# Optimization experiments

Measured on AMD Instinct MI355X. Metric: run time of the kernel, lower is better.

## Reference

```python
import jax, jax.numpy as jnp
import numpy as np

# --- LCAModel hyperparameters (from init_kwargs) ---
NUM_SIMS = 2048
NUM_DIM = 8
NUM_STEPS = 1500
THRESHOLD = 1.0
LEAK = 0.1
COMPETITION = 0.1
SELF_EXC = 0.0
NOISE_STD = 1.0
DT = 0.01
SQRT_STEP = float(np.sqrt(0.001))  # hardcoded in LCALayer (sqrt(0.001), not sqrt(DT))


def setup_inputs() -> dict:
    key = jax.random.key(0)
    inp = jax.random.uniform(key, (NUM_SIMS, NUM_DIM), dtype=jnp.float32)
    return {"input": inp}


def reference(input):
    B, D = input.shape
    # gamma: off-diagonal -competition, diagonal self_excitation
    gamma = jnp.full((D, D), -COMPETITION, dtype=input.dtype)
    gamma = gamma.at[jnp.diag_indices(D)].set(SELF_EXC)
    noise_key = jax.random.key(42)

    def step(carry, t):
        pre, act = carry
        # stop integrating once any accumulator crosses threshold
        active = jnp.all(jnp.abs(act) < THRESHOLD, axis=1, keepdims=True).astype(pre.dtype)
        # faithful to torch: sum(matmul(act, gamma), dim=1, keepdim=True) -> [B, 1]
        rec = jnp.sum(act @ gamma, axis=1, keepdims=True)
        pre = pre + (input - LEAK * pre + rec) * active * DT
        dw = active * NOISE_STD * jax.random.normal(
            jax.random.fold_in(noise_key, t), (B, D), dtype=pre.dtype)
        pre = pre + dw * SQRT_STEP
        act = jax.nn.relu(pre)
        return (pre, act), (pre, act)

    init = (jnp.zeros_like(input), jnp.zeros_like(input))
    _, (pre_traj, act_traj) = jax.lax.scan(step, init, jnp.arange(NUM_STEPS))
    # prepend the zero initial state and move time to the last axis: [B, D, T+1]
    zeros = jnp.zeros((1, B, D), input.dtype)
    pre_all = jnp.moveaxis(jnp.concatenate([zeros, pre_traj], axis=0), 0, -1)
    act_all = jnp.moveaxis(jnp.concatenate([zeros, act_traj], axis=0), 0, -1)
    return (pre_all, act_all)
```

## Files before the change

kernel.cpp:

```cpp
#include <hip/hip_runtime.h>
#include <stdint.h>

#define NSIMS 2048
#define NDIM 8
#define NE (NSIMS * NDIM)
#define NSTEPS 1500
#define TP1 (NSTEPS + 1)
#define TILE 64
#define NTILE ((NSTEPS + TILE - 1) / TILE)
#define SENT 0x7fffffff

__device__ __forceinline__ void tf_block(uint32_t k0, uint32_t k1,
                                         uint32_t x0, uint32_t x1,
                                         uint32_t& o0, uint32_t& o1) {
  const uint32_t k2 = k0 ^ k1 ^ 0x1BD11BDAu;
  x0 += k0; x1 += k1;
#define TF_R(r) { x0 += x1; x1 = (x1 << (r)) | (x1 >> (32 - (r))); x1 ^= x0; }
  TF_R(13) TF_R(15) TF_R(26) TF_R(6)
  x0 += k1; x1 += k2 + 1u;
  TF_R(17) TF_R(29) TF_R(16) TF_R(24)
  x0 += k2; x1 += k0 + 2u;
  TF_R(13) TF_R(15) TF_R(26) TF_R(6)
  x0 += k0; x1 += k1 + 3u;
  TF_R(17) TF_R(29) TF_R(16) TF_R(24)
  x0 += k1; x1 += k2 + 4u;
  TF_R(13) TF_R(15) TF_R(26) TF_R(6)
  x0 += k2; x1 += k0 + 5u;
#undef TF_R
  o0 = x0; o1 = x1;
}

__device__ __forceinline__ float bits_to_normal(uint32_t bits) {
#pragma clang fp contract(off)
  const float LO = -0.99999994f;
  float f = __uint_as_float((bits >> 9) | 0x3F800000u) - 1.0f;
  float u = f * 2.0f + LO;
  u = fmaxf(LO, u);
  float t = __builtin_fmaf(-u, u, 1.0f);
  float L = __log2f(t);
  float p;
  if (L > -7.2134752f) {
    float w = __builtin_fmaf(-0.69314718f, L, -2.5f);
    p = 3.97426059e-08f;
    p = 4.85462660e-07f + p * w;
    p = -4.98282379e-06f + p * w;
    p = -6.21053119e-06f + p * w;
    p = 3.09120051e-04f + p * w;
    p = -1.77303519e-03f + p * w;
    p = -5.90813402e-03f + p * w;
    p = 3.48802730e-01f + p * w;
    p = 2.12331454e+00f + p * w;
  } else {
    float w = sqrtf(-0.69314718f * L) - 3.0f;
    p = -2.83145880e-04f;
    p = 1.42765648e-04f + p * w;
    p = 1.90826058e-03f + p * w;
    p = -5.19501312e-03f + p * w;
    p = 8.11688966e-03f + p * w;
    p = -1.07797881e-02f + p * w;
    p = 1.33485786e-02f + p * w;
    p = 1.41658104e+00f + p * w;
    p = 4.00643424e+00f + p * w;
  }
  return p * u;
}

__global__ void k_fold(uint2* __restrict__ keys) {
  int t = blockIdx.x * blockDim.x + threadIdx.x;
  if (t >= NSTEPS) return;
  uint32_t o0, o1;
  tf_block(0u, 42u, 0u, (uint32_t)t, o0, o1);
  keys[t] = make_uint2(o0, o1);
}

template <int CTRL>
__device__ __forceinline__ float dppf(float v) {
  int r = __builtin_amdgcn_update_dpp(0, __builtin_bit_cast(int, v), CTRL, 0xF, 0xF, true);
  return __builtin_bit_cast(float, r);
}
template <int CTRL>
__device__ __forceinline__ int dppi(int v) {
  return __builtin_amdgcn_update_dpp(0, v, CTRL, 0xF, 0xF, true);
}

#define STEP(ST, NZ)                                                    \
  {                                                                     \
    _Pragma("clang fp contract(off)")                                   \
    float S = act;                                                      \
    S = S + dppf<0xB1>(S);                                              \
    S = S + dppf<0x4E>(S);                                              \
    S = S + dppf<0x141>(S);                                             \
    const float rec = (S * -0.1f) * 7.0f;   \
    float a_ = inp - 0.1f * pre;                                        \
    float b_ = a_ + rec;                                                \
    float cg = b_ * activeF;                                            \
    pre = pre + cg * 0.01f;                                             \
    float dwn = activeF * (NZ);                                         \
    pre = pre + dwn * 0.031622776601683793f; \
    act = fmaxf(pre, 0.0f);                                             \
    fc = (act >= 1.0f) ? (((ST) < fc) ? (ST) : fc) : fc;                \
    ptile[ST][lane] = pre;                                              \
  }

__global__ void __launch_bounds__(512, 2) k_fused(const float* __restrict__ input,
                                                  const uint2* __restrict__ keys,
                                                  float* __restrict__ out) {
  __shared__ float ring[2][TILE][64];
  __shared__ float ptile[TILE][65];
  __shared__ float spre[64];
  __shared__ int sfz;
  const int tid = threadIdx.x;
  const int wid = tid >> 6;
  const int lane = tid & 63;
  const int e0 = (int)blockIdx.x << 6;
  const int e = e0 + lane;
  const size_t actoff = (size_t)NE * TP1;

  if (tid == 0) sfz = SENT;

  float pre = 0.0f, act = 0.0f, activeF = 1.0f, inp = 0.0f;
  if (wid == 0) {
    inp = input[e];
    const size_t rowo = (size_t)e * TP1;
    out[rowo] = 0.0f;
    out[actoff + rowo] = 0.0f;
  } else {
    const int j0 = wid - 1;
    uint2 fk[10];
#pragma unroll
    for (int rr = 0; rr < 10; ++rr) {
      const int j = j0 + rr * 7;
      fk[rr] = (j < TILE) ? keys[j] : make_uint2(0u, 0u);
    }
#pragma unroll
    for (int rr = 0; rr < 10; ++rr) {
      const int j = j0 + rr * 7;
      if (j < TILE) {
        uint32_t o0, o1;
        tf_block(fk[rr].x, fk[rr].y, 0u, (uint32_t)e, o0, o1);
        ring[0][j][lane] = bits_to_normal(o0 ^ o1);
      }
    }
  }
  __syncthreads();

  int fz = SENT;
  for (int k = 0; k < NTILE; ++k) {
    const int par = k & 1;
    const int base = k * TILE;
    const int nst = (NSTEPS - base < TILE) ? (NSTEPS - base) : TILE;
    if (wid == 0) {
      int fc = TILE;
      if (nst == TILE) {
#pragma unroll
        for (int ch = 0; ch < 2; ++ch) {
          float nz[32];
#pragma unroll
          for (int j = 0; j < 32; ++j) nz[j] = ring[par][ch * 32 + j][lane];
#pragma unroll
          for (int j = 0; j < 32; ++j) STEP(ch * 32 + j, nz[j])
        }
      } else {
#pragma unroll
        for (int ch = 0; ch < 2; ++ch) {
          float nz[32];
#pragma unroll
          for (int j = 0; j < 32; ++j) nz[j] = ring[par][ch * 32 + j][lane];
#pragma unroll
          for (int j = 0; j < 32; ++j) {
            const int st = ch * 32 + j;
            if (st >= nst) break;
            STEP(st, nz[j])
          }
        }
      }
      int c = fc;
      { int t_ = dppi<0xB1>(c);  c = (t_ < c) ? t_ : c; }
      { int t_ = dppi<0x4E>(c);  c = (t_ < c) ? t_ : c; }
      { int t_ = dppi<0x141>(c); c = (t_ < c) ? t_ : c; }
      if (activeF > 0.0f && c < TILE) {
        const float fpre = ptile[c][lane];
        for (int s = c + 1; s < TILE; ++s) ptile[s][lane] = fpre;
        pre = fpre;
        act = fmaxf(fpre, 0.0f);
        activeF = 0.0f;
      }
      if (__ballot(activeF > 0.0f) == 0ull) {
        spre[lane] = pre;
        if (lane == 0) sfz = base + nst + 1;
      }
    } else {
      const int nb = base + TILE;
      const int j0 = wid - 1;
      uint2 fk[10];
#pragma unroll
      for (int rr = 0; rr < 10; ++rr) {
        const int j = j0 + rr * 7;
        const int t = nb + j;
        fk[rr] = (j < TILE && t < NSTEPS) ? keys[t] : make_uint2(0u, 0u);
      }
#pragma unroll
      for (int rr = 0; rr < 10; ++rr) {
        const int j = j0 + rr * 7;
        const int t = nb + j;
        if (j < TILE && t < NSTEPS) {
          uint32_t o0, o1;
          tf_block(fk[rr].x, fk[rr].y, 0u, (uint32_t)e, o0, o1);
          ring[par ^ 1][j][lane] = bits_to_normal(o0 ^ o1);
        }
      }
    }
    __syncthreads();
    if (lane < nst) {
      const int tau = base + 1 + lane;
#pragma unroll
      for (int ee = 0; ee < 8; ++ee) {
        const int el = (wid << 3) + ee;
        const float p = ptile[lane][el];
        const size_t o = (size_t)(e0 + el) * TP1 + (size_t)tau;
        out[o] = p;
        out[actoff + o] = fmaxf(p, 0.0f);
      }
    }
    if (sfz != SENT) { fz = sfz; break; }
    __syncthreads();
  }

  if (fz <= NSTEPS) {
#pragma unroll
    for (int ee = 0; ee < 8; ++ee) {
      const int el = (wid << 3) + ee;
      const float p = spre[el];
      const float a = fmaxf(p, 0.0f);
      const size_t ro = (size_t)(e0 + el) * TP1;
      for (int tau = fz + lane; tau <= NSTEPS; tau += 64) {
        out[ro + (size_t)tau] = p;
        out[actoff + ro + (size_t)tau] = a;
      }
    }
  }
}

extern "C" void kernel_launch(void* const* d_in, const int* in_sizes, int n_in,
                              void* d_out, int out_size, void* d_ws, size_t ws_size,
                              hipStream_t stream) {
  const float* input = (const float*)d_in[0];
  float* out = (float*)d_out;
  uint2* keys = (uint2*)d_ws;
  if (ws_size < NSTEPS * sizeof(uint2)) return;

  k_fold<<<dim3((NSTEPS + 255) / 256), dim3(256), 0, stream>>>(keys);
  k_fused<<<dim3(NSIMS / 8), dim3(512), 0, stream>>>(input, keys, out);
}
```

Baseline: 128.4 us.

## Double tile size, shorten reduction chain, and drop active-mask from recurrence

Raises the time tile from 64 to 128 steps, which halves the number of block-wide barriers and tile handoffs. The 8-lane sum is rebuilt as a shallower DPP tree with parallel adds, which shortens the serial dependency chain of each step. The active mask is removed from the per-step update: frozen lanes keep integrating, and the store phase overwrites their output with the frozen value using shared sfroz/spre flags. The noise-generation loops become rolled with a key prefetch, and the launch bound drops the minimum-2-blocks hint. The larger shared-memory footprint and the looser register limit may reduce occupancy, and the reordered additions may change rounding relative to the sequential sum.

```diff
diff --git a/kernel.cpp b/kernel.cpp
--- a/kernel.cpp
+++ b/kernel.cpp
@@ -6,7 +6,7 @@
 #define NE (NSIMS * NDIM)
 #define NSTEPS 1500
 #define TP1 (NSTEPS + 1)
-#define TILE 64
+#define TILE 128
 #define NTILE ((NSTEPS + TILE - 1) / TILE)
 #define SENT 0x7fffffff
 
@@ -86,28 +86,30 @@
 #define STEP(ST, NZ)                                                    \
   {                                                                     \
     _Pragma("clang fp contract(off)")                                   \
-    float S = act;                                                      \
-    S = S + dppf<0xB1>(S);                                              \
-    S = S + dppf<0x4E>(S);                                              \
-    S = S + dppf<0x141>(S);                                             \
+    float x1 = dppf<0xB1>(act);                                         \
+    float x2 = dppf<0x4E>(act);                                         \
+    float x3 = dppf<0x1B>(act);                                         \
+    float t1 = act + x1;                                                \
+    float t2 = x2 + x3;                                                 \
+    float Q = t1 + t2;                                                  \
+    float S = Q + dppf<0x141>(Q);                                       \
     const float rec = (S * -0.1f) * 7.0f;   \
     float a_ = inp - 0.1f * pre;                                        \
     float b_ = a_ + rec;                                                \
-    float cg = b_ * activeF;                                            \
-    pre = pre + cg * 0.01f;                                             \
-    float dwn = activeF * (NZ);                                         \
-    pre = pre + dwn * 0.031622776601683793f; \
+    pre = pre + b_ * 0.01f;                                             \
+    pre = pre + (NZ) * 0.031622776601683793f;   \
     act = fmaxf(pre, 0.0f);                                             \
     fc = (act >= 1.0f) ? (((ST) < fc) ? (ST) : fc) : fc;                \
     ptile[ST][lane] = pre;                                              \
   }
 
-__global__ void __launch_bounds__(512, 2) k_fused(const float* __restrict__ input,
-                                                  const uint2* __restrict__ keys,
-                                                  float* __restrict__ out) {
+__global__ void __launch_bounds__(512) k_fused(const float* __restrict__ input,
+                                               const uint2* __restrict__ keys,
+                                               float* __restrict__ out) {
   __shared__ float ring[2][TILE][64];
   __shared__ float ptile[TILE][65];
   __shared__ float spre[64];
+  __shared__ float sfroz[64];
   __shared__ int sfz;
   const int tid = threadIdx.x;
   const int wid = tid >> 6;
@@ -118,28 +120,23 @@
 
   if (tid == 0) sfz = SENT;
 
-  float pre = 0.0f, act = 0.0f, activeF = 1.0f, inp = 0.0f;
+  float pre = 0.0f, act = 0.0f, inp = 0.0f, spreR = 0.0f;
+  int actv = 1;
   if (wid == 0) {
     inp = input[e];
     const size_t rowo = (size_t)e * TP1;
     out[rowo] = 0.0f;
     out[actoff + rowo] = 0.0f;
   } else {
-    const int j0 = wid - 1;
-    uint2 fk[10];
-#pragma unroll
-    for (int rr = 0; rr < 10; ++rr) {
-      const int j = j0 + rr * 7;
-      fk[rr] = (j < TILE) ? keys[j] : make_uint2(0u, 0u);
-    }
-#pragma unroll
-    for (int rr = 0; rr < 10; ++rr) {
-      const int j = j0 + rr * 7;
-      if (j < TILE) {
-        uint32_t o0, o1;
-        tf_block(fk[rr].x, fk[rr].y, 0u, (uint32_t)e, o0, o1);
-        ring[0][j][lane] = bits_to_normal(o0 ^ o1);
-      }
+    int j = wid - 1;
+    uint2 fk = keys[j];
+    for (; j < TILE; j += 7) {
+      const int jn = j + 7;
+      uint2 fkn = (jn < TILE) ? keys[jn] : fk;
+      uint32_t o0, o1;
+      tf_block(fk.x, fk.y, 0u, (uint32_t)e, o0, o1);
+      ring[0][j][lane] = bits_to_normal(o0 ^ o1);
+      fk = fkn;
     }
   }
   __syncthreads();
@@ -150,10 +147,12 @@
     const int base = k * TILE;
     const int nst = (NSTEPS - base < TILE) ? (NSTEPS - base) : TILE;
     if (wid == 0) {
+      sfroz[lane] = actv ? 0.0f : 1.0f;
+      spre[lane] = spreR;
       int fc = TILE;
       if (nst == TILE) {
-#pragma unroll
-        for (int ch = 0; ch < 2; ++ch) {
+#pragma unroll 1
+        for (int ch = 0; ch < TILE / 32; ++ch) {
           float nz[32];
 #pragma unroll
           for (int j = 0; j < 32; ++j) nz[j] = ring[par][ch * 32 + j][lane];
@@ -161,8 +160,8 @@
           for (int j = 0; j < 32; ++j) STEP(ch * 32 + j, nz[j])
         }
       } else {
-#pragma unroll
-        for (int ch = 0; ch < 2; ++ch) {
+#pragma unroll 1
+        for (int ch = 0; ch < TILE / 32; ++ch) {
           float nz[32];
 #pragma unroll
           for (int j = 0; j < 32; ++j) nz[j] = ring[par][ch * 32 + j][lane];
@@ -178,48 +177,55 @@
       { int t_ = dppi<0xB1>(c);  c = (t_ < c) ? t_ : c; }
       { int t_ = dppi<0x4E>(c);  c = (t_ < c) ? t_ : c; }
       { int t_ = dppi<0x141>(c); c = (t_ < c) ? t_ : c; }
-      if (activeF > 0.0f && c < TILE) {
+      if (actv && c < TILE) {
         const float fpre = ptile[c][lane];
         for (int s = c + 1; s < TILE; ++s) ptile[s][lane] = fpre;
-        pre = fpre;
-        act = fmaxf(fpre, 0.0f);
-        activeF = 0.0f;
-      }
-      if (__ballot(activeF > 0.0f) == 0ull) {
-        spre[lane] = pre;
+        spreR = fpre;
+        actv = 0;
+      }
+      if (__ballot(actv != 0) == 0ull) {
+        spre[lane] = spreR;
         if (lane == 0) sfz = base + nst + 1;
       }
     } else {
       const int nb = base + TILE;
-      const int j0 = wid - 1;
-      uint2 fk[10];
-#pragma unroll
-      for (int rr = 0; rr < 10; ++rr) {
-        const int j = j0 + rr * 7;
-        const int t = nb + j;
-        fk[rr] = (j < TILE && t < NSTEPS) ? keys[t] : make_uint2(0u, 0u);
-      }
-#pragma unroll
-      for (int rr = 0; rr < 10; ++rr) {
-        const int j = j0 + rr * 7;
-        const int t = nb + j;
-        if (j < TILE && t < NSTEPS) {
+      int j = wid - 1;
+      if (nb + j < NSTEPS) {
+        uint2 fk = keys[nb + j];
+        for (; j < TILE && nb + j < NSTEPS; j += 7) {
+          const int tn = nb + j + 7;
+          uint2 fkn = (j + 7 < TILE && tn < NSTEPS) ? keys[tn] : fk;
           uint32_t o0, o1;
-          tf_block(fk[rr].x, fk[rr].y, 0u, (uint32_t)e, o0, o1);
+          tf_block(fk.x, fk.y, 0u, (uint32_t)e, o0, o1);
           ring[par ^ 1][j][lane] = bits_to_normal(o0 ^ o1);
+          fk = fkn;
         }
       }
     }
     __syncthreads();
-    if (lane < nst) {
-      const int tau = base + 1 + lane;
+    {
+      float fm[8], sv[8];
 #pragma unroll
       for (int ee = 0; ee < 8; ++ee) {
         const int el = (wid << 3) + ee;
-        const float p = ptile[lane][el];
-        const size_t o = (size_t)(e0 + el) * TP1 + (size_t)tau;
-        out[o] = p;
-        out[actoff + o] = fmaxf(p, 0.0f);
+        fm[ee] = sfroz[el];
+        sv[ee] = spre[el];
+      }
+#pragma unroll
+      for (int tb = 0; tb < TILE / 64; ++tb) {
+        const int ln = nst - tb * 64;
+        if (lane < ln) {
+          const int tau = base + 1 + tb * 64 + lane;
+#pragma unroll
+          for (int ee = 0; ee < 8; ++ee) {
+            const int el = (wid << 3) + ee;
+            float p = ptile[tb * 64 + lane][el];
+            p = (fm[ee] > 0.0f) ? sv[ee] : p;
+            const size_t o = (size_t)(e0 + el) * TP1 + (size_t)tau;
+            out[o] = p;
+            out[actoff + o] = fmaxf(p, 0.0f);
+          }
+        }
       }
     }
     if (sfz != SENT) { fz = sfz; break; }
```

New measurement: 134.1 us (median of 2 runs). 1.04x slower.
